# Performance work log

Hardware: AMD Instinct MI355X
Metric: run time of the kernel (lower is better)

Reference implementation:

```python
import jax, jax.numpy as jnp
import numpy as np
from jax import lax

NB_DIGITS = 2
BASE = 10
NUMS = BASE ** NB_DIGITS            # 100 possible values per number
SUMS = 2 * (NUMS - 1) + 1           # 199 possible sums (circuit roots)
B = 4096                            # logical batch size
N_IMAGES = B * 2 * NB_DIGITS        # 16384 digit images


def setup_inputs() -> dict:
    key = jax.random.key(0)
    ks = jax.random.split(key, 11)
    s = 0.1
    return {
        "images": jax.random.normal(ks[0], (N_IMAGES, 1, 28, 28), jnp.float32),
        "conv1_w": jax.random.normal(ks[1], (6, 1, 5, 5), jnp.float32) * s,
        "conv1_b": jax.random.normal(ks[2], (6,), jnp.float32) * s,
        "conv2_w": jax.random.normal(ks[3], (16, 6, 5, 5), jnp.float32) * s,
        "conv2_b": jax.random.normal(ks[4], (16,), jnp.float32) * s,
        "fc1_w": jax.random.normal(ks[5], (120, 256), jnp.float32) * s,
        "fc1_b": jax.random.normal(ks[6], (120,), jnp.float32) * s,
        "fc2_w": jax.random.normal(ks[7], (84, 120), jnp.float32) * s,
        "fc2_b": jax.random.normal(ks[8], (84,), jnp.float32) * s,
        "fc3_w": jax.random.normal(ks[9], (10, 84), jnp.float32) * s,
        "fc3_b": jax.random.normal(ks[10], (10,), jnp.float32) * s,
    }


def _conv(x, w, b):
    y = lax.conv_general_dilated(x, w, (1, 1), 'VALID',
                                 dimension_numbers=('NCHW', 'OIHW', 'NCHW'))
    return y + b[None, :, None, None]


def _maxpool2(x):
    return lax.reduce_window(x, -jnp.inf, lax.max, (1, 1, 2, 2), (1, 1, 2, 2), 'VALID')


def _lenet(x, c1w, c1b, c2w, c2b, f1w, f1b, f2w, f2b, f3w, f3b):
    x = jax.nn.relu(_maxpool2(_conv(x, c1w, c1b)))   # [N,6,12,12]
    x = jax.nn.relu(_maxpool2(_conv(x, c2w, c2b)))   # [N,16,4,4]
    x = x.reshape(-1, 16 * 4 * 4)
    x = jax.nn.relu(x @ f1w.T + f1b)
    x = jax.nn.relu(x @ f2w.T + f2b)
    x = x @ f3w.T + f3b
    return jax.nn.log_softmax(x, axis=-1)            # [N,10]


def _circuit(lp):
    # lp: [B, 2*NB_DIGITS, 10] per-digit log-probs.
    # Vars layout from get_circuit: positions 0..NB_DIGITS-1 = n1 digits (MSB first),
    # positions NB_DIGITS..2*NB_DIGITS-1 = n2 digits. Neg-literal weights are 0 in
    # log space (the `zeros` arg), so each model's weight = sum of digit log-probs;
    # OR over models = logsumexp grouped by n1+n2.
    d = jnp.arange(NUMS)
    hi, lo = d // BASE, d % BASE
    lp1 = lp[:, 0, hi] + lp[:, 1, lo]                # [B, NUMS] log P(n1=k)
    lp2 = lp[:, 2, hi] + lp[:, 3, lo]                # [B, NUMS] log P(n2=k)
    M = (lp1[:, :, None] + lp2[:, None, :]).reshape(lp.shape[0], -1)  # [B, NUMS^2]
    seg = (jnp.arange(NUMS)[:, None] + jnp.arange(NUMS)[None, :]).reshape(-1)
    Mf = M.T                                          # [NUMS^2, B]
    m = jax.ops.segment_max(Mf, seg, num_segments=SUMS)              # [SUMS, B]
    ssum = jax.ops.segment_sum(jnp.exp(Mf - m[seg]), seg, num_segments=SUMS)
    return (jnp.log(ssum) + m).T                      # [B, SUMS] log P(sum=s)


def reference(images, conv1_w, conv1_b, conv2_w, conv2_b,
              fc1_w, fc1_b, fc2_w, fc2_b, fc3_w, fc3_b):
    logp = _lenet(images, conv1_w, conv1_b, conv2_w, conv2_b,
                  fc1_w, fc1_b, fc2_w, fc2_b, fc3_w, fc3_b)   # [N_IMAGES,10]
    lp = logp.reshape(B, 2 * NB_DIGITS, BASE)
    return _circuit(lp)
```

## Files before the change

### kernel.cpp

```cpp
#include <hip/hip_runtime.h>
#include <hip/hip_bf16.h>
#include <math.h>

#define SUMS 199
#define NBLK 1024

typedef __attribute__((ext_vector_type(8))) short short8;
typedef __attribute__((ext_vector_type(4))) float float4v;

union Frag8 { short8 v; unsigned u[4]; uint4 q; };

static __device__ inline unsigned pk_bf16(float a, float b) {
    __hip_bfloat162 h = __float22bfloat162_rn(make_float2(a, b));
    union { __hip_bfloat162 h; unsigned u; } c; c.h = h; return c.u;
}
static __device__ inline unsigned short bf16_1(float a) {
    union { __hip_bfloat16 h; unsigned short u; } c;
    c.h = __float2bfloat16(a); return c.u;
}
template <int CTRL>
static __device__ inline float fmax_xdpp(float v) {
    const int s = __builtin_amdgcn_update_dpp(0, __float_as_int(v), CTRL, 0xF, 0xF, true);
    return fmaxf(v, __int_as_float(s));
}
template <int CTRL>
static __device__ inline float add_xdpp(float v) {
    const int s = __builtin_amdgcn_update_dpp(0, __float_as_int(v), CTRL, 0xF, 0xF, true);
    return v + __int_as_float(s);
}

__global__ __launch_bounds__(256) void convert_weights(
    const float* __restrict__ f1w, const float* __restrict__ f2w,
    const float* __restrict__ f3w, const float* __restrict__ c1w,
    const float* __restrict__ c2w, uint4* __restrict__ ws)
{
    const int g = blockIdx.x * 256 + threadIdx.x;
    if (g >= 6400) return;
    float v[8];
    if (g < 5824) {
        const float* W; int O, K, ld, nt, s, l;
        if (g < 4096)      { W = f1w; O = 120; K = 256; ld = 256; nt = g >> 9; s = (g >> 6) & 7; l = g & 63; }
        else if (g < 5632) { const int f = g - 4096; W = f2w; O = 84; K = 120; ld = 120; nt = f >> 8; s = (f >> 6) & 3; l = f & 63; }
        else               { const int f = g - 5632; W = f3w; O = 10; K = 84;  ld = 84;  nt = 0; s = f >> 6; l = f & 63; }
        const int o = nt * 16 + (l & 15);
        #pragma unroll
        for (int j = 0; j < 8; ++j) {
            const int k = 32 * s + 8 * (l >> 4) + j;
            v[j] = (o < O && k < K) ? W[o * ld + k] : 0.f;
        }
    } else if (g < 6336) {
        const int f = g - 5824, s = f >> 6, l = f & 63;
        const int c = l & 15, h = l >> 4;
        const int pos = 4 * s + h;
        const int ky = pos / 5, kx = pos % 5;
        const bool ok = (pos < 25);
        #pragma unroll
        for (int jp = 0; jp < 4; ++jp) {
            v[2 * jp]     = (ok && 2 * jp < 6)     ? c2w[c * 150 + (2 * jp) * 25 + ky * 5 + kx]     : 0.f;
            v[2 * jp + 1] = (ok && 2 * jp + 1 < 6) ? c2w[c * 150 + (2 * jp + 1) * 25 + ky * 5 + kx] : 0.f;
        }
    } else {
        const int l = (g - 6336) & 63;
        const int c = l & 15, h = l >> 4;
        const int oc = c >> 1, xs = c & 1;
        #pragma unroll
        for (int j = 0; j < 8; ++j) {
            const int p = h * 4 + (j >> 1);
            float w = 0.f;
            if (p < 15 && c < 12) {
                const int ky = p / 3, kx = 2 * (p % 3) + (j & 1) - xs;
                if (kx >= 0 && kx < 5) w = c1w[oc * 25 + ky * 5 + kx];
            }
            v[j] = w;
        }
    }
    uint4 r;
    r.x = pk_bf16(v[0], v[1]); r.y = pk_bf16(v[2], v[3]);
    r.z = pk_bf16(v[4], v[5]); r.w = pk_bf16(v[6], v[7]);
    ws[g] = r;
}

__global__ __launch_bounds__(256, 4) void lenet_circuit_kernel(
    const float* __restrict__ images,
    const float* __restrict__ c1b, const float* __restrict__ c2b,
    const float* __restrict__ f1b, const float* __restrict__ f2b,
    const float* __restrict__ f3b, const uint4* __restrict__ wsb,
    float* __restrict__ out)
{
    __shared__ __align__(16) unsigned char s_mem[39680];
    unsigned*       imgu = (unsigned*)s_mem;
    uint2*          imgw = (uint2*)s_mem;
    unsigned short* p1s  = (unsigned short*)(s_mem + 12672);
    const uint4*    p1u4 = (const uint4*)(s_mem + 12672);
    unsigned short* A1s  = (unsigned short*)(s_mem + 31232);
    const uint4*    A1q  = (const uint4*)(s_mem + 31232);
    float*          pgf  = (float*)(s_mem + 7680);
    float*          Hf   = (float*)(s_mem + 8448);
    float*          Lf   = (float*)(s_mem + 8768);

    const int t = threadIdx.x, bid = blockIdx.x;
    const int lane = t & 63, wav = t >> 6;
    const int c = lane & 15, h = lane >> 4;
    const uint4 z4 = {0u, 0u, 0u, 0u};

    const int qxo = c >> 2, parity = (c >> 1) & 1, irel = c & 1;

    {
        uint4* pz = (uint4*)(s_mem + 12672) + 2 * wav * 145;
        for (int j = lane; j < 290; j += 64) pz[j] = z4;
    }
    Frag8 a1; a1.q = wsb[6336 + lane];
    Frag8 w2[7];
    #pragma unroll
    for (int s = 0; s < 7; ++s) w2[s].q = wsb[5824 + s * 64 + lane];
    int koff[7];
    #pragma unroll
    for (int s = 0; s < 7; ++s) {
        const int pos = 4 * s + h;
        koff[s] = (pos < 25) ? (pos / 5) * 12 + (pos % 5) : 0;
    }
    int pd[4];
    #pragma unroll
    for (int q = 0; q < 4; ++q) {
        const int p = 4 * h + q;
        pd[q] = (p < 15) ? (p / 3) * 14 + (p % 3) : 0;
    }
    float bias0 = 0.f, bias1 = 0.f;
    if (h < 3) { bias0 = c1b[2 * h]; bias1 = c1b[2 * h + 1]; }
    const float b2v = c2b[c];

    float4 pf[7];
    {
        const float4* g1 = (const float4*)(images + (size_t)bid * 12544 + 6272) + 392 * wav;
        #pragma unroll
        for (int k = 0; k < 7; ++k) {
            const int i = lane + 64 * k;
            if (i < 392) pf[k] = g1[i];
        }
    }

    auto do_stage1 = [&]() {
        #pragma unroll
        for (int k = 0; k < 7; ++k) {
            const int i = lane + 64 * k;
            if (i < 392) {
                const int im = 2 * wav + (i >= 196);
                const int j = i - ((i >= 196) ? 196 : 0);
                uint2 wv; wv.x = pk_bf16(pf[k].x, pf[k].y); wv.y = pk_bf16(pf[k].z, pf[k].w);
                imgw[im * 198 + j] = wv;
            }
        }
    };
    auto do_conv1 = [&]() {
        const int img = 2 * wav + irel;
        const int imb = img * 396 + parity * 14 + qxo;
        const int pst = img * 1160 + 2 * h;
        unsigned dA[12], dB[12];
        #pragma unroll
        for (int x = 0; x < 3; ++x)
            #pragma unroll
            for (int q = 0; q < 4; ++q)
                dA[x * 4 + q] = imgu[imb + x * 4 + pd[q]];
        #pragma unroll
        for (int qy = 0; qy < 12; ++qy) {
            const unsigned* cur = (qy & 1) ? dB : dA;
            unsigned*       nxt = (qy & 1) ? dA : dB;
            if (qy < 11) {
                const int nb = imb + (qy + 1) * 28;
                #pragma unroll
                for (int x = 0; x < 3; ++x)
                    #pragma unroll
                    for (int q = 0; q < 4; ++q)
                        nxt[x * 4 + q] = imgu[nb + x * 4 + pd[q]];
            }
            float4v acc[3];
            #pragma unroll
            for (int x = 0; x < 3; ++x) {
                Frag8 bf;
                #pragma unroll
                for (int q = 0; q < 4; ++q) bf.u[q] = cur[x * 4 + q];
                float4v a0 = {0.f, 0.f, 0.f, 0.f};
                acc[x] = __builtin_amdgcn_mfma_f32_16x16x32_bf16(a1.v, bf.v, a0, 0, 0, 0);
            }
            float v0[3], v1[3];
            #pragma unroll
            for (int x = 0; x < 3; ++x) {
                v0[x] = fmax_xdpp<0x4E>(fmaxf(acc[x][0], acc[x][1]));
                v1[x] = fmax_xdpp<0x4E>(fmaxf(acc[x][2], acc[x][3]));
            }
            if (parity == 0 && h < 3) {
                #pragma unroll
                for (int x = 0; x < 3; ++x) {
                    const int qx = x * 4 + qxo;
                    *(unsigned*)&p1s[pst + qy * 96 + qx * 8] =
                        pk_bf16(fmaxf(v0[x] + bias0, 0.f), fmaxf(v1[x] + bias1, 0.f));
                }
            }
        }
    };
    auto do_conv2 = [&](int pass) {
        const int pxl = (c & 1) + 2 * ((c >> 2) & 1);
        const int pyl = ((c >> 1) & 1) + 2 * ((c >> 3) & 1);
        #pragma unroll
        for (int ii = 0; ii < 2; ++ii) {
            const int i0 = 2 * wav + ii;
            float ov[4];
            #pragma unroll
            for (int mt = 0; mt < 4; ++mt) {
                const int base = i0 * 145 + (pyl + 4 * (mt >> 1)) * 12 + pxl + 4 * (mt & 1);
                uint4 r[7];
                #pragma unroll
                for (int s = 0; s < 7; ++s) r[s] = p1u4[base + koff[s]];
                float4v acc = {0.f, 0.f, 0.f, 0.f};
                #pragma unroll
                for (int s = 0; s < 7; ++s) {
                    Frag8 af; af.q = r[s];
                    acc = __builtin_amdgcn_mfma_f32_16x16x32_bf16(af.v, w2[s].v, acc, 0, 0, 0);
                }
                const float p = fmaxf(fmaxf(acc[0], acc[1]), fmaxf(acc[2], acc[3]));
                ov[mt] = fmaxf(p + b2v, 0.f);
            }
            const int img = pass * 8 + i0;
            #pragma unroll
            for (int mt = 0; mt < 4; ++mt) {
                const int qy = (h >> 1) + 2 * (mt >> 1);
                A1s[img * 264 + c * 16 + qy * 4 + 2 * (mt & 1) + (h & 1)] = bf16_1(ov[mt]);
            }
        }
    };

    {
        const float4* g = (const float4*)(images + (size_t)bid * 12544) + 392 * wav;
        #pragma unroll
        for (int k = 0; k < 7; ++k) {
            const int i = lane + 64 * k;
            if (i < 392) {
                const float4 v = g[i];
                const int im = 2 * wav + (i >= 196);
                const int j = i - ((i >= 196) ? 196 : 0);
                uint2 wv; wv.x = pk_bf16(v.x, v.y); wv.y = pk_bf16(v.z, v.w);
                imgw[im * 198 + j] = wv;
            }
        }
    }
    do_conv1();
    do_stage1();
    do_conv2(0);
    do_conv1();
    do_conv2(1);

    const int nt0 = 2 * wav;
    Frag8 fB0[4], fB1[4];
    #pragma unroll
    for (int s = 0; s < 4; ++s) {
        fB0[s].q = wsb[(nt0 * 8 + s) * 64 + lane];
        fB1[s].q = wsb[((nt0 + 1) * 8 + s) * 64 + lane];
    }
    __syncthreads();

    {
        unsigned* A2d = (unsigned*)s_mem;
        unsigned short* A2s = (unsigned short*)s_mem;
        if (t < 64) A2d[(t >> 2) * 68 + 60 + (t & 3)] = 0u;
        Frag8 gB0[4], gB1[4];
        #pragma unroll
        for (int s = 0; s < 4; ++s) {
            gB0[s].q = wsb[(nt0 * 8 + 4 + s) * 64 + lane];
            gB1[s].q = wsb[((nt0 + 1) * 8 + 4 + s) * 64 + lane];
        }
        Frag8 afA[4];
        #pragma unroll
        for (int s = 0; s < 4; ++s) afA[s].q = A1q[c * 33 + 4 * s + h];
        float4v acc0 = {0.f, 0.f, 0.f, 0.f}, acc1 = acc0;
        #pragma unroll
        for (int s = 0; s < 4; ++s) {
            acc0 = __builtin_amdgcn_mfma_f32_16x16x32_bf16(afA[s].v, fB0[s].v, acc0, 0, 0, 0);
            acc1 = __builtin_amdgcn_mfma_f32_16x16x32_bf16(afA[s].v, fB1[s].v, acc1, 0, 0, 0);
        }
        #pragma unroll
        for (int s = 0; s < 4; ++s) afA[s].q = A1q[c * 33 + 4 * (4 + s) + h];
        #pragma unroll
        for (int s = 0; s < 4; ++s) {
            acc0 = __builtin_amdgcn_mfma_f32_16x16x32_bf16(afA[s].v, gB0[s].v, acc0, 0, 0, 0);
            acc1 = __builtin_amdgcn_mfma_f32_16x16x32_bf16(afA[s].v, gB1[s].v, acc1, 0, 0, 0);
        }
        #pragma unroll
        for (int ntl = 0; ntl < 2; ++ntl) {
            const int o = 32 * wav + 16 * ntl + c;
            if (o < 120) {
                const float bias = f1b[o];
                #pragma unroll
                for (int r = 0; r < 4; ++r) {
                    const float v = fmaxf((ntl ? acc1[r] : acc0[r]) + bias, 0.f);
                    A2s[(4 * h + r) * 136 + o] = bf16_1(v);
                }
            }
        }
    }
    Frag8 hB0[4], hB1[4];
    if (wav < 3) {
        #pragma unroll
        for (int s = 0; s < 4; ++s) {
            hB0[s].q = wsb[4096 + (nt0 * 4 + s) * 64 + lane];
            hB1[s].q = wsb[4096 + ((nt0 + 1) * 4 + s) * 64 + lane];
        }
    }
    __syncthreads();

    {
        unsigned* A3d = (unsigned*)(s_mem + 4352);
        unsigned short* A3s = (unsigned short*)(s_mem + 4352);
        if (t < 96) A3d[(t / 6) * 52 + 42 + (t % 6)] = 0u;
        if (wav < 3) {
            const uint4* A2q = (const uint4*)s_mem;
            Frag8 afA[4];
            #pragma unroll
            for (int s = 0; s < 4; ++s) afA[s].q = A2q[c * 17 + 4 * s + h];
            float4v acc0 = {0.f, 0.f, 0.f, 0.f}, acc1 = acc0;
            #pragma unroll
            for (int s = 0; s < 4; ++s) {
                acc0 = __builtin_amdgcn_mfma_f32_16x16x32_bf16(afA[s].v, hB0[s].v, acc0, 0, 0, 0);
                acc1 = __builtin_amdgcn_mfma_f32_16x16x32_bf16(afA[s].v, hB1[s].v, acc1, 0, 0, 0);
            }
            #pragma unroll
            for (int ntl = 0; ntl < 2; ++ntl) {
                const int o = 32 * wav + 16 * ntl + c;
                if (o < 84) {
                    const float bias = f2b[o];
                    #pragma unroll
                    for (int r = 0; r < 4; ++r) {
                        const float v = fmaxf((ntl ? acc1[r] : acc0[r]) + bias, 0.f);
                        A3s[(4 * h + r) * 104 + o] = bf16_1(v);
                    }
                }
            }
        }
    }
    Frag8 tB[3];
    #pragma unroll
    for (int s = 0; s < 3; ++s) tB[s].q = wsb[5632 + s * 64 + lane];
    __syncthreads();

    {
        const uint4* A3q = (const uint4*)(s_mem + 4352);
        Frag8 afA[3];
        #pragma unroll
        for (int s = 0; s < 3; ++s) afA[s].q = A3q[c * 13 + 4 * s + h];
        float4v acc = {0.f, 0.f, 0.f, 0.f};
        #pragma unroll
        for (int s = 0; s < 3; ++s)
            acc = __builtin_amdgcn_mfma_f32_16x16x32_bf16(afA[s].v, tB[s].v, acc, 0, 0, 0);
        const float bias = (c < 10) ? f3b[c] : 0.f;
        float x[4], m[4], e[4], sm[4];
        #pragma unroll
        for (int r = 0; r < 4; ++r) {
            x[r] = (c < 10) ? (acc[r] + bias) : -INFINITY;
            m[r] = x[r];
        }
        #pragma unroll
        for (int r = 0; r < 4; ++r) m[r] = fmax_xdpp<0xB1>(m[r]);
        #pragma unroll
        for (int r = 0; r < 4; ++r) m[r] = fmax_xdpp<0x4E>(m[r]);
        #pragma unroll
        for (int d = 4; d <= 8; d <<= 1)
            #pragma unroll
            for (int r = 0; r < 4; ++r) m[r] = fmaxf(m[r], __shfl_xor(m[r], d));
        #pragma unroll
        for (int r = 0; r < 4; ++r) { e[r] = (c < 10) ? expf(x[r] - m[r]) : 0.f; sm[r] = e[r]; }
        #pragma unroll
        for (int r = 0; r < 4; ++r) sm[r] = add_xdpp<0xB1>(sm[r]);
        #pragma unroll
        for (int r = 0; r < 4; ++r) sm[r] = add_xdpp<0x4E>(sm[r]);
        #pragma unroll
        for (int d = 4; d <= 8; d <<= 1)
            #pragma unroll
            for (int r = 0; r < 4; ++r) sm[r] += __shfl_xor(sm[r], d);
        if (c < 10 && h == wav) {
            #pragma unroll
            for (int r = 0; r < 4; ++r)
                pgf[(4 * wav + r) * 12 + c] = e[r] / sm[r];
        }

        if (lane < 38) {
            const int isH = (lane < 19), b = isH ? lane : lane - 19;
            const float* pg = pgf + 4 * wav * 12;
            const float* PA = pg + (isH ? 0 : 12);
            const float* PB = pg + (isH ? 24 : 36);
            const int ilo = (b > 9) ? b - 9 : 0;
            const int ihi = (b < 9) ? b : 9;
            float s = 0.f;
            for (int i = ilo; i <= ihi; ++i) s += PA[i] * PB[b - i];
            (isH ? Hf : Lf)[wav * 20 + b] = s;
        }

        const float* H = Hf + wav * 20;
        const float* L = Lf + wav * 20;
        for (int s = lane; s < SUMS; s += 64) {
            const int bmin = (s > 18) ? (s - 9) / 10 : 0;
            int bmax = s / 10; if (bmax > 18) bmax = 18;
            float sum = 0.f;
            for (int b = bmin; b <= bmax; ++b) sum += H[b] * L[s - 10 * b];
            out[((size_t)bid * 4 + wav) * SUMS + s] = logf(sum);
        }
    }
}

extern "C" void kernel_launch(void* const* d_in, const int* in_sizes, int n_in,
                              void* d_out, int out_size, void* d_ws, size_t ws_size,
                              hipStream_t stream) {
    const float* images = (const float*)d_in[0];
    const float* c1w = (const float*)d_in[1];
    const float* c1b = (const float*)d_in[2];
    const float* c2w = (const float*)d_in[3];
    const float* c2b = (const float*)d_in[4];
    const float* f1w = (const float*)d_in[5];
    const float* f1b = (const float*)d_in[6];
    const float* f2w = (const float*)d_in[7];
    const float* f2b = (const float*)d_in[8];
    const float* f3w = (const float*)d_in[9];
    const float* f3b = (const float*)d_in[10];
    float* out = (float*)d_out;

    convert_weights<<<25, 256, 0, stream>>>(f1w, f2w, f3w, c1w, c2w, (uint4*)d_ws);
    lenet_circuit_kernel<<<NBLK, 256, 0, stream>>>(
        images, c1b, c2b, f1b, f2b, f3b, (const uint4*)d_ws, out);
}
```

Baseline: 128.2 us.

## Use 512-thread blocks with one image per wave per pass

Doubles the block to 8 waves so each wave handles one image per pass instead of two, restructures conv1 to process row pairs without double-buffering, and interleaves conv2 across four M-tiles per weight step, loading weights from global inside the loop. The FC layers are split so each wave computes one 16-column tile, and the final layer and circuit stage run only on the first four waves. It also swaps expf/logf for the fast intrinsics. The aim is more waves in flight and more independent MFMA chains, at the cost of higher per-block register and occupancy demands (launch bounds 512,8) and idle waves in the tail stages.

```diff
diff --git a/kernel.cpp b/kernel.cpp
--- a/kernel.cpp
+++ b/kernel.cpp
@@ -80,7 +80,7 @@
     ws[g] = r;
 }
 
-__global__ __launch_bounds__(256, 4) void lenet_circuit_kernel(
+__global__ __launch_bounds__(512, 8) void lenet_circuit_kernel(
     const float* __restrict__ images,
     const float* __restrict__ c1b, const float* __restrict__ c2b,
     const float* __restrict__ f1b, const float* __restrict__ f2b,
@@ -103,16 +103,13 @@
     const int c = lane & 15, h = lane >> 4;
     const uint4 z4 = {0u, 0u, 0u, 0u};
 
-    const int qxo = c >> 2, parity = (c >> 1) & 1, irel = c & 1;
+    const int qxo = c >> 2, par = (c >> 1) & 1, qyo = c & 1;
 
     {
-        uint4* pz = (uint4*)(s_mem + 12672) + 2 * wav * 145;
-        for (int j = lane; j < 290; j += 64) pz[j] = z4;
+        uint4* pz = (uint4*)(s_mem + 12672) + wav * 145;
+        for (int j = lane; j < 145; j += 64) pz[j] = z4;
     }
     Frag8 a1; a1.q = wsb[6336 + lane];
-    Frag8 w2[7];
-    #pragma unroll
-    for (int s = 0; s < 7; ++s) w2[s].q = wsb[5824 + s * 64 + lane];
     int koff[7];
     #pragma unroll
     for (int s = 0; s < 7; ++s) {
@@ -129,181 +126,123 @@
     if (h < 3) { bias0 = c1b[2 * h]; bias1 = c1b[2 * h + 1]; }
     const float b2v = c2b[c];
 
-    float4 pf[7];
-    {
-        const float4* g1 = (const float4*)(images + (size_t)bid * 12544 + 6272) + 392 * wav;
-        #pragma unroll
-        for (int k = 0; k < 7; ++k) {
-            const int i = lane + 64 * k;
-            if (i < 392) pf[k] = g1[i];
-        }
-    }
-
-    auto do_stage1 = [&]() {
-        #pragma unroll
-        for (int k = 0; k < 7; ++k) {
-            const int i = lane + 64 * k;
-            if (i < 392) {
-                const int im = 2 * wav + (i >= 196);
-                const int j = i - ((i >= 196) ? 196 : 0);
-                uint2 wv; wv.x = pk_bf16(pf[k].x, pf[k].y); wv.y = pk_bf16(pf[k].z, pf[k].w);
-                imgw[im * 198 + j] = wv;
-            }
-        }
-    };
-    auto do_conv1 = [&]() {
-        const int img = 2 * wav + irel;
-        const int imb = img * 396 + parity * 14 + qxo;
-        const int pst = img * 1160 + 2 * h;
-        unsigned dA[12], dB[12];
-        #pragma unroll
-        for (int x = 0; x < 3; ++x)
-            #pragma unroll
-            for (int q = 0; q < 4; ++q)
-                dA[x * 4 + q] = imgu[imb + x * 4 + pd[q]];
-        #pragma unroll
-        for (int qy = 0; qy < 12; ++qy) {
-            const unsigned* cur = (qy & 1) ? dB : dA;
-            unsigned*       nxt = (qy & 1) ? dA : dB;
-            if (qy < 11) {
-                const int nb = imb + (qy + 1) * 28;
+    #pragma unroll
+    for (int pass = 0; pass < 2; ++pass) {
+        {
+            const float4* g = (const float4*)(images) +
+                              ((size_t)bid * 16 + pass * 8 + wav) * 196;
+            #pragma unroll
+            for (int k = 0; k < 4; ++k) {
+                const int i = lane + 64 * k;
+                if (i < 196) {
+                    const float4 v = g[i];
+                    uint2 wv; wv.x = pk_bf16(v.x, v.y); wv.y = pk_bf16(v.z, v.w);
+                    imgw[wav * 198 + i] = wv;
+                }
+            }
+        }
+        {
+            const int imb = wav * 396 + (2 * qyo + par) * 14 + qxo;
+            const int pst = wav * 1160 + 2 * h;
+            for (int Q = 0; Q < 6; ++Q) {
+                unsigned d[12];
                 #pragma unroll
                 for (int x = 0; x < 3; ++x)
                     #pragma unroll
                     for (int q = 0; q < 4; ++q)
-                        nxt[x * 4 + q] = imgu[nb + x * 4 + pd[q]];
-            }
-            float4v acc[3];
-            #pragma unroll
-            for (int x = 0; x < 3; ++x) {
-                Frag8 bf;
-                #pragma unroll
-                for (int q = 0; q < 4; ++q) bf.u[q] = cur[x * 4 + q];
-                float4v a0 = {0.f, 0.f, 0.f, 0.f};
-                acc[x] = __builtin_amdgcn_mfma_f32_16x16x32_bf16(a1.v, bf.v, a0, 0, 0, 0);
-            }
-            float v0[3], v1[3];
-            #pragma unroll
-            for (int x = 0; x < 3; ++x) {
-                v0[x] = fmax_xdpp<0x4E>(fmaxf(acc[x][0], acc[x][1]));
-                v1[x] = fmax_xdpp<0x4E>(fmaxf(acc[x][2], acc[x][3]));
-            }
-            if (parity == 0 && h < 3) {
+                        d[x * 4 + q] = imgu[imb + Q * 56 + x * 4 + pd[q]];
+                float4v acc[3];
                 #pragma unroll
                 for (int x = 0; x < 3; ++x) {
-                    const int qx = x * 4 + qxo;
-                    *(unsigned*)&p1s[pst + qy * 96 + qx * 8] =
-                        pk_bf16(fmaxf(v0[x] + bias0, 0.f), fmaxf(v1[x] + bias1, 0.f));
-                }
-            }
-        }
-    };
-    auto do_conv2 = [&](int pass) {
-        const int pxl = (c & 1) + 2 * ((c >> 2) & 1);
-        const int pyl = ((c >> 1) & 1) + 2 * ((c >> 3) & 1);
-        #pragma unroll
-        for (int ii = 0; ii < 2; ++ii) {
-            const int i0 = 2 * wav + ii;
-            float ov[4];
+                    Frag8 bf;
+                    #pragma unroll
+                    for (int q = 0; q < 4; ++q) bf.u[q] = d[x * 4 + q];
+                    float4v a0 = {0.f, 0.f, 0.f, 0.f};
+                    acc[x] = __builtin_amdgcn_mfma_f32_16x16x32_bf16(a1.v, bf.v, a0, 0, 0, 0);
+                }
+                float v0[3], v1[3];
+                #pragma unroll
+                for (int x = 0; x < 3; ++x) {
+                    v0[x] = fmax_xdpp<0x4E>(fmaxf(acc[x][0], acc[x][1]));
+                    v1[x] = fmax_xdpp<0x4E>(fmaxf(acc[x][2], acc[x][3]));
+                }
+                if (par == 0 && h < 3) {
+                    #pragma unroll
+                    for (int x = 0; x < 3; ++x) {
+                        const int qy = 2 * Q + qyo, qx = x * 4 + qxo;
+                        *(unsigned*)&p1s[pst + qy * 96 + qx * 8] =
+                            pk_bf16(fmaxf(v0[x] + bias0, 0.f), fmaxf(v1[x] + bias1, 0.f));
+                    }
+                }
+            }
+        }
+        {
+            const int pxl = (c & 1) + 2 * ((c >> 2) & 1);
+            const int pyl = ((c >> 1) & 1) + 2 * ((c >> 3) & 1);
+            int pbase[4];
+            #pragma unroll
+            for (int mt = 0; mt < 4; ++mt)
+                pbase[mt] = wav * 145 + (pyl + 4 * (mt >> 1)) * 12 + pxl + 4 * (mt & 1);
+            float4v acc[4];
+            #pragma unroll
+            for (int mt = 0; mt < 4; ++mt) acc[mt] = (float4v){0.f, 0.f, 0.f, 0.f};
+            #pragma unroll
+            for (int s = 0; s < 7; ++s) {
+                Frag8 wz; wz.q = wsb[5824 + s * 64 + lane];
+                #pragma unroll
+                for (int mt = 0; mt < 4; ++mt) {
+                    Frag8 af; af.q = p1u4[pbase[mt] + koff[s]];
+                    acc[mt] = __builtin_amdgcn_mfma_f32_16x16x32_bf16(af.v, wz.v, acc[mt], 0, 0, 0);
+                }
+            }
+            const int img = pass * 8 + wav;
             #pragma unroll
             for (int mt = 0; mt < 4; ++mt) {
-                const int base = i0 * 145 + (pyl + 4 * (mt >> 1)) * 12 + pxl + 4 * (mt & 1);
-                uint4 r[7];
-                #pragma unroll
-                for (int s = 0; s < 7; ++s) r[s] = p1u4[base + koff[s]];
-                float4v acc = {0.f, 0.f, 0.f, 0.f};
-                #pragma unroll
-                for (int s = 0; s < 7; ++s) {
-                    Frag8 af; af.q = r[s];
-                    acc = __builtin_amdgcn_mfma_f32_16x16x32_bf16(af.v, w2[s].v, acc, 0, 0, 0);
-                }
-                const float p = fmaxf(fmaxf(acc[0], acc[1]), fmaxf(acc[2], acc[3]));
-                ov[mt] = fmaxf(p + b2v, 0.f);
-            }
-            const int img = pass * 8 + i0;
-            #pragma unroll
-            for (int mt = 0; mt < 4; ++mt) {
+                const float p = fmaxf(fmaxf(acc[mt][0], acc[mt][1]),
+                                      fmaxf(acc[mt][2], acc[mt][3]));
+                const float ov = fmaxf(p + b2v, 0.f);
                 const int qy = (h >> 1) + 2 * (mt >> 1);
-                A1s[img * 264 + c * 16 + qy * 4 + 2 * (mt & 1) + (h & 1)] = bf16_1(ov[mt]);
-            }
-        }
-    };
-
-    {
-        const float4* g = (const float4*)(images + (size_t)bid * 12544) + 392 * wav;
-        #pragma unroll
-        for (int k = 0; k < 7; ++k) {
-            const int i = lane + 64 * k;
-            if (i < 392) {
-                const float4 v = g[i];
-                const int im = 2 * wav + (i >= 196);
-                const int j = i - ((i >= 196) ? 196 : 0);
-                uint2 wv; wv.x = pk_bf16(v.x, v.y); wv.y = pk_bf16(v.z, v.w);
-                imgw[im * 198 + j] = wv;
-            }
-        }
-    }
-    do_conv1();
-    do_stage1();
-    do_conv2(0);
-    do_conv1();
-    do_conv2(1);
-
-    const int nt0 = 2 * wav;
-    Frag8 fB0[4], fB1[4];
+                A1s[img * 264 + c * 16 + qy * 4 + 2 * (mt & 1) + (h & 1)] = bf16_1(ov);
+            }
+        }
+    }
+
+    Frag8 fB[4];
     #pragma unroll
-    for (int s = 0; s < 4; ++s) {
-        fB0[s].q = wsb[(nt0 * 8 + s) * 64 + lane];
-        fB1[s].q = wsb[((nt0 + 1) * 8 + s) * 64 + lane];
-    }
+    for (int s = 0; s < 4; ++s) fB[s].q = wsb[(wav * 8 + s) * 64 + lane];
     __syncthreads();
 
     {
         unsigned* A2d = (unsigned*)s_mem;
         unsigned short* A2s = (unsigned short*)s_mem;
         if (t < 64) A2d[(t >> 2) * 68 + 60 + (t & 3)] = 0u;
-        Frag8 gB0[4], gB1[4];
-        #pragma unroll
-        for (int s = 0; s < 4; ++s) {
-            gB0[s].q = wsb[(nt0 * 8 + 4 + s) * 64 + lane];
-            gB1[s].q = wsb[((nt0 + 1) * 8 + 4 + s) * 64 + lane];
-        }
+        Frag8 gB[4];
+        #pragma unroll
+        for (int s = 0; s < 4; ++s) gB[s].q = wsb[(wav * 8 + 4 + s) * 64 + lane];
         Frag8 afA[4];
         #pragma unroll
         for (int s = 0; s < 4; ++s) afA[s].q = A1q[c * 33 + 4 * s + h];
-        float4v acc0 = {0.f, 0.f, 0.f, 0.f}, acc1 = acc0;
-        #pragma unroll
-        for (int s = 0; s < 4; ++s) {
-            acc0 = __builtin_amdgcn_mfma_f32_16x16x32_bf16(afA[s].v, fB0[s].v, acc0, 0, 0, 0);
-            acc1 = __builtin_amdgcn_mfma_f32_16x16x32_bf16(afA[s].v, fB1[s].v, acc1, 0, 0, 0);
-        }
+        float4v acc = {0.f, 0.f, 0.f, 0.f};
+        #pragma unroll
+        for (int s = 0; s < 4; ++s)
+            acc = __builtin_amdgcn_mfma_f32_16x16x32_bf16(afA[s].v, fB[s].v, acc, 0, 0, 0);
         #pragma unroll
         for (int s = 0; s < 4; ++s) afA[s].q = A1q[c * 33 + 4 * (4 + s) + h];
         #pragma unroll
-        for (int s = 0; s < 4; ++s) {
-            acc0 = __builtin_amdgcn_mfma_f32_16x16x32_bf16(afA[s].v, gB0[s].v, acc0, 0, 0, 0);
-            acc1 = __builtin_amdgcn_mfma_f32_16x16x32_bf16(afA[s].v, gB1[s].v, acc1, 0, 0, 0);
-        }
-        #pragma unroll
-        for (int ntl = 0; ntl < 2; ++ntl) {
-            const int o = 32 * wav + 16 * ntl + c;
-            if (o < 120) {
-                const float bias = f1b[o];
-                #pragma unroll
-                for (int r = 0; r < 4; ++r) {
-                    const float v = fmaxf((ntl ? acc1[r] : acc0[r]) + bias, 0.f);
-                    A2s[(4 * h + r) * 136 + o] = bf16_1(v);
-                }
-            }
-        }
-    }
-    Frag8 hB0[4], hB1[4];
-    if (wav < 3) {
-        #pragma unroll
-        for (int s = 0; s < 4; ++s) {
-            hB0[s].q = wsb[4096 + (nt0 * 4 + s) * 64 + lane];
-            hB1[s].q = wsb[4096 + ((nt0 + 1) * 4 + s) * 64 + lane];
-        }
+        for (int s = 0; s < 4; ++s)
+            acc = __builtin_amdgcn_mfma_f32_16x16x32_bf16(afA[s].v, gB[s].v, acc, 0, 0, 0);
+        const int o = 16 * wav + c;
+        if (o < 120) {
+            const float bias = f1b[o];
+            #pragma unroll
+            for (int r = 0; r < 4; ++r)
+                A2s[(4 * h + r) * 136 + o] = bf16_1(fmaxf(acc[r] + bias, 0.f));
+        }
+    }
+    Frag8 hB[4];
+    if (wav < 6) {
+        #pragma unroll
+        for (int s = 0; s < 4; ++s) hB[s].q = wsb[4096 + (wav * 4 + s) * 64 + lane];
     }
     __syncthreads();
 
@@ -311,37 +250,32 @@
         unsigned* A3d = (unsigned*)(s_mem + 4352);
         unsigned short* A3s = (unsigned short*)(s_mem + 4352);
         if (t < 96) A3d[(t / 6) * 52 + 42 + (t % 6)] = 0u;
-        if (wav < 3) {
+        if (wav < 6) {
             const uint4* A2q = (const uint4*)s_mem;
             Frag8 afA[4];
             #pragma unroll
             for (int s = 0; s < 4; ++s) afA[s].q = A2q[c * 17 + 4 * s + h];
-            float4v acc0 = {0.f, 0.f, 0.f, 0.f}, acc1 = acc0;
-            #pragma unroll
-            for (int s = 0; s < 4; ++s) {
-                acc0 = __builtin_amdgcn_mfma_f32_16x16x32_bf16(afA[s].v, hB0[s].v, acc0, 0, 0, 0);
-                acc1 = __builtin_amdgcn_mfma_f32_16x16x32_bf16(afA[s].v, hB1[s].v, acc1, 0, 0, 0);
-            }
-            #pragma unroll
-            for (int ntl = 0; ntl < 2; ++ntl) {
-                const int o = 32 * wav + 16 * ntl + c;
-                if (o < 84) {
-                    const float bias = f2b[o];
-                    #pragma unroll
-                    for (int r = 0; r < 4; ++r) {
-                        const float v = fmaxf((ntl ? acc1[r] : acc0[r]) + bias, 0.f);
-                        A3s[(4 * h + r) * 104 + o] = bf16_1(v);
-                    }
-                }
+            float4v acc = {0.f, 0.f, 0.f, 0.f};
+            #pragma unroll
+            for (int s = 0; s < 4; ++s)
+                acc = __builtin_amdgcn_mfma_f32_16x16x32_bf16(afA[s].v, hB[s].v, acc, 0, 0, 0);
+            const int o = 16 * wav + c;
+            if (o < 84) {
+                const float bias = f2b[o];
+                #pragma unroll
+                for (int r = 0; r < 4; ++r)
+                    A3s[(4 * h + r) * 104 + o] = bf16_1(fmaxf(acc[r] + bias, 0.f));
             }
         }
     }
     Frag8 tB[3];
-    #pragma unroll
-    for (int s = 0; s < 3; ++s) tB[s].q = wsb[5632 + s * 64 + lane];
+    if (wav < 4) {
+        #pragma unroll
+        for (int s = 0; s < 3; ++s) tB[s].q = wsb[5632 + s * 64 + lane];
+    }
     __syncthreads();
 
-    {
+    if (wav < 4) {
         const uint4* A3q = (const uint4*)(s_mem + 4352);
         Frag8 afA[3];
         #pragma unroll
@@ -366,7 +300,7 @@
             #pragma unroll
             for (int r = 0; r < 4; ++r) m[r] = fmaxf(m[r], __shfl_xor(m[r], d));
         #pragma unroll
-        for (int r = 0; r < 4; ++r) { e[r] = (c < 10) ? expf(x[r] - m[r]) : 0.f; sm[r] = e[r]; }
+        for (int r = 0; r < 4; ++r) { e[r] = (c < 10) ? __expf(x[r] - m[r]) : 0.f; sm[r] = e[r]; }
         #pragma unroll
         for (int r = 0; r < 4; ++r) sm[r] = add_xdpp<0xB1>(sm[r]);
         #pragma unroll
@@ -400,7 +334,7 @@
             int bmax = s / 10; if (bmax > 18) bmax = 18;
             float sum = 0.f;
             for (int b = bmin; b <= bmax; ++b) sum += H[b] * L[s - 10 * b];
-            out[((size_t)bid * 4 + wav) * SUMS + s] = logf(sum);
+            out[((size_t)bid * 4 + wav) * SUMS + s] = __logf(sum);
         }
     }
 }
@@ -422,6 +356,6 @@
     float* out = (float*)d_out;
 
     convert_weights<<<25, 256, 0, stream>>>(f1w, f2w, f3w, c1w, c2w, (uint4*)d_ws);
-    lenet_circuit_kernel<<<NBLK, 256, 0, stream>>>(
+    lenet_circuit_kernel<<<NBLK, 512, 0, stream>>>(
         images, c1b, c2b, f1b, f2b, f3b, (const uint4*)d_ws, out);
 }
```

Measured after the change: 129.1 us. No clear change (+0.7%).
